# Optimization experiments

Hardware: AMD Instinct MI355X
Metric: run time of the kernel (lower is better)

The kernel has to match this reference:

```python
import jax, jax.numpy as jnp
import numpy as np

N_TOKENS = 65536
HIDDEN = 1024
N_EXPERTS = 64
EPS = 1e-12  # matches F.normalize default eps
NEG_BIG = float(jnp.finfo(jnp.bfloat16).max)  # -torch.finfo(bfloat16).max sentinel


def setup_inputs() -> dict:
    key = jax.random.key(0)
    k1, k2 = jax.random.split(key)
    x = jax.random.normal(k1, (N_TOKENS, HIDDEN), dtype=jnp.float32)
    sim_matrix = jax.random.normal(k2, (HIDDEN, N_EXPERTS), dtype=jnp.float32)  # nn.Parameter(randn)
    gates = jnp.zeros((N_EXPERTS,), dtype=jnp.float32)  # nn.Parameter(zeros)
    return {"x": x, "sim_matrix": sim_matrix, "gates": gates}


def _l2norm(v, axis):
    n = jnp.sqrt(jnp.sum(v * v, axis=axis, keepdims=True))
    return v / jnp.maximum(n, EPS)


def reference(x, sim_matrix, gates):
    # cosine-similarity logits: [N, E]
    logits = jnp.matmul(_l2norm(x, -1), _l2norm(sim_matrix, 0))
    thr = jax.nn.sigmoid(gates)                      # [E]
    pre_activation_logits = logits - thr             # [N, E]
    gated = jax.nn.relu(pre_activation_logits)
    # STE: forward hard 0/1, backward identity
    hard = (gated > 0).astype(x.dtype)
    activation_mask = gated + jax.lax.stop_gradient(hard - gated)
    # topk fallback for rows with zero active experts (vectorized scatter)
    inactive = jnp.sum(hard, axis=1) == 0            # [N]
    k_fallback = N_EXPERTS // 2
    _, topk_idx = jax.lax.top_k(logits, k_fallback)  # [N, k]
    rows = jnp.arange(x.shape[0])
    fb = jnp.zeros_like(logits).at[rows[:, None], topk_idx].set(1.0)
    activation_mask = jnp.where(inactive[:, None], fb, activation_mask)
    # masked softmax over active experts
    masked = jnp.where(activation_mask > 0, gated, -NEG_BIG)
    active_expert_probs = jax.nn.softmax(masked, axis=-1)
    return active_expert_probs, pre_activation_logits, activation_mask
```

## Files before the change

kernel.cpp:

```cpp
#include <hip/hip_runtime.h>
#include <math.h>

#define N_TOK   65536
#define HID     1024
#define NEXP    64
#define EPSF    1e-12f
#define EPSW    4e-5f

typedef __attribute__((ext_vector_type(8))) short s16x8;
typedef __attribute__((ext_vector_type(4))) float f32x4;

__device__ __forceinline__ unsigned short f2bf(float f) {
    unsigned u = __float_as_uint(f);
    unsigned r = u + 0x7fffu + ((u >> 16) & 1u);
    return (unsigned short)(r >> 16);
}
__device__ __forceinline__ float bf2f(unsigned short h) {
    return __uint_as_float(((unsigned)h) << 16);
}
__device__ __forceinline__ unsigned enc_key(float f) {
    unsigned u = __float_as_uint(f);
    return (u & 0x80000000u) ? ~u : (u | 0x80000000u);
}
__device__ __forceinline__ float dec_key(unsigned k) {
    unsigned u = (k & 0x80000000u) ? (k ^ 0x80000000u) : ~k;
    return __uint_as_float(u);
}

__global__ __launch_bounds__(256) void prep_kernel(const float* __restrict__ sim,
                                                   const float* __restrict__ gates,
                                                   float* __restrict__ ws) {
    __shared__ float partial[4][64];
    int e = threadIdx.x & 63;
    int q = threadIdx.x >> 6;
    float s = 0.f;
    for (int h = q * 256; h < q * 256 + 256; ++h) {
        float v = sim[h * NEXP + e];
        s += v * v;
    }
    partial[q][e] = s;
    __syncthreads();
    if (threadIdx.x < 64) {
        float ss = partial[0][e] + partial[1][e] + partial[2][e] + partial[3][e];
        ws[e] = 1.0f / fmaxf(sqrtf(ss), EPSF);
        ws[64 + e] = 1.0f / (1.0f + expf(-gates[e]));
    }
}

__global__ __launch_bounds__(256) void prep2n_kernel(const float* __restrict__ sim,
                                                     const float* __restrict__ ws_ro,
                                                     float* __restrict__ wn) {
    int idx = blockIdx.x * 256 + threadIdx.x;
    wn[idx] = sim[idx] * ws_ro[idx & 63];
}

__global__ __launch_bounds__(256) void prep3_kernel(const float* __restrict__ wn,
                                                    unsigned short* __restrict__ wbh,
                                                    unsigned short* __restrict__ wbl) {
    int i = blockIdx.x * 256 + threadIdx.x;
    int j    = i & 7;
    int lane = (i >> 3) & 63;
    int nt   = (i >> 9) & 3;
    int kt   = i >> 11;
    int k = kt * 32 + ((lane >> 4) & 3) * 8 + j;
    int e = nt * 16 + (lane & 15);
    float v = wn[k * NEXP + e];
    unsigned short h = f2bf(v);
    unsigned short l = f2bf(v - bf2f(h));
    wbh[i] = h; wbl[i] = l;
}

__global__ __launch_bounds__(256) void gate_v11_kernel(const float* __restrict__ x,
                                                       const float* __restrict__ wn,
                                                       const unsigned short* __restrict__ wbh,
                                                       const unsigned short* __restrict__ wbl,
                                                       const float* __restrict__ prep,
                                                       float* __restrict__ out) {
    __shared__ __align__(16) float smem[6016];
    float* xrow    = smem + 4352;
    float* ss_part = smem + 5376;
    float* thr_l   = smem + 5632;
    int*   flags_i = (int*)(smem + 5696);
    float* part    = smem + 5760;
    unsigned short* AhU = (unsigned short*)smem;
    unsigned short* AlU = (unsigned short*)(smem + 2080);

    const int tid   = threadIdx.x;
    const int lane  = tid & 63;
    const int wv    = tid >> 6;
    const int tbase = blockIdx.x * 64;

    const int t_st = tid & 63;
    const int q_st = tid >> 6;
    const int fl   = (t_st & 15) + 16 * q_st;
    const int mt   = t_st >> 4;
    const float* xrow_g = x + (size_t)(tbase + t_st) * HID;

    if (tid < 64) thr_l[tid] = prep[64 + tid];

    f32x4 acc[4];
#pragma unroll
    for (int m = 0; m < 4; ++m) acc[m] = (f32x4){0.f, 0.f, 0.f, 0.f};
    float ss = 0.f;

    const s16x8* bh_g = (const s16x8*)wbh;
    const s16x8* bl_g = (const s16x8*)wbl;

    {
        float4 v0 = *(const float4*)(xrow_g + q_st * 8);
        float4 v1 = *(const float4*)(xrow_g + q_st * 8 + 4);
        const float a[8] = { v0.x, v0.y, v0.z, v0.w, v1.x, v1.y, v1.z, v1.w };
        s16x8 hv, lv;
#pragma unroll
        for (int i = 0; i < 8; ++i) {
            ss = fmaf(a[i], a[i], ss);
            unsigned short h = f2bf(a[i]);
            hv[i] = (short)h;
            lv[i] = (short)f2bf(a[i] - bf2f(h));
        }
        int slot = mt * 65 + fl;
        *(s16x8*)&AhU[slot * 8] = hv;
        *(s16x8*)&AlU[slot * 8] = lv;
    }
    s16x8 bh = bh_g[(0 * 4 + wv) * 64 + lane];
    s16x8 bl = bl_g[(0 * 4 + wv) * 64 + lane];
    __syncthreads();

#pragma unroll 1
    for (int c = 0; c < 32; ++c) {
        const int buf = c & 1;
        float4 nv0, nv1;
        s16x8 nbh, nbl;
        if (c < 31) {
            nv0 = *(const float4*)(xrow_g + (c + 1) * 32 + q_st * 8);
            nv1 = *(const float4*)(xrow_g + (c + 1) * 32 + q_st * 8 + 4);
            nbh = bh_g[((c + 1) * 4 + wv) * 64 + lane];
            nbl = bl_g[((c + 1) * 4 + wv) * 64 + lane];
        }

        s16x8 ah[4], al[4];
#pragma unroll
        for (int m = 0; m < 4; ++m) {
            int base = ((buf << 2) + m) * 65 * 8 + lane * 8;
            ah[m] = *(const s16x8*)&AhU[base];
            al[m] = *(const s16x8*)&AlU[base];
        }
#pragma unroll
        for (int m = 0; m < 4; ++m)
            acc[m] = __builtin_amdgcn_mfma_f32_16x16x32_bf16(al[m], bh, acc[m], 0, 0, 0);
#pragma unroll
        for (int m = 0; m < 4; ++m)
            acc[m] = __builtin_amdgcn_mfma_f32_16x16x32_bf16(ah[m], bl, acc[m], 0, 0, 0);
#pragma unroll
        for (int m = 0; m < 4; ++m)
            acc[m] = __builtin_amdgcn_mfma_f32_16x16x32_bf16(ah[m], bh, acc[m], 0, 0, 0);

        if (c < 31) {
            const float a[8] = { nv0.x, nv0.y, nv0.z, nv0.w, nv1.x, nv1.y, nv1.z, nv1.w };
            s16x8 hv, lv;
#pragma unroll
            for (int i = 0; i < 8; ++i) {
                ss = fmaf(a[i], a[i], ss);
                unsigned short h = f2bf(a[i]);
                hv[i] = (short)h;
                lv[i] = (short)f2bf(a[i] - bf2f(h));
            }
            int slot = (((buf ^ 1) << 2) + mt) * 65 + fl;
            *(s16x8*)&AhU[slot * 8] = hv;
            *(s16x8*)&AlU[slot * 8] = lv;
            bh = nbh; bl = nbl;
        }
        __syncthreads();
    }

    ss_part[q_st * 64 + t_st] = ss;
    {
        float* lg = smem;
#pragma unroll
        for (int m = 0; m < 4; ++m) {
#pragma unroll
            for (int r = 0; r < 4; ++r) {
                int tok = m * 16 + (lane >> 4) * 4 + r;
                int e   = wv * 16 + (lane & 15);
                lg[tok * 68 + e] = acc[m][r];
            }
        }
    }
    __syncthreads();

    const int tg = lane >> 3;
    const int eg = lane & 7;
    const int e0 = eg * 8;
    const size_t out_pre  = (size_t)N_TOK * NEXP;
    const size_t out_mask = 2 * (size_t)N_TOK * NEXP;

#pragma unroll
    for (int j = 0; j < 2; ++j) {
        const int tl = wv * 16 + tg * 2 + j;
        const int t  = tbase + tl;
        const float sst = (ss_part[tl] + ss_part[64 + tl])
                        + (ss_part[128 + tl] + ss_part[192 + tl]);
        const float inv = 1.0f / fmaxf(sqrtf(sst), EPSF);

        float logit[8], pre[8];
        int active[8];
        int myact = 0;
#pragma unroll
        for (int i = 0; i < 8; ++i) {
            logit[i] = smem[tl * 68 + e0 + i] * inv;
            pre[i]   = logit[i] - thr_l[e0 + i];
            active[i] = pre[i] > 0.f;
            myact += active[i];
        }
        *(float4*)&out[out_pre + (size_t)t * NEXP + e0]     = make_float4(pre[0], pre[1], pre[2], pre[3]);
        *(float4*)&out[out_pre + (size_t)t * NEXP + e0 + 4] = make_float4(pre[4], pre[5], pre[6], pre[7]);

        int rowact = myact;
        rowact += __shfl_xor(rowact, 1, 8);
        rowact += __shfl_xor(rowact, 2, 8);
        rowact += __shfl_xor(rowact, 4, 8);

        int flag;
        if (rowact > 0) {
            float mn = 1e30f;
#pragma unroll
            for (int i = 0; i < 8; ++i) mn = fminf(mn, fabsf(pre[i]));
            mn = fminf(mn, __shfl_xor(mn, 1, 8));
            mn = fminf(mn, __shfl_xor(mn, 2, 8));
            mn = fminf(mn, __shfl_xor(mn, 4, 8));
            flag = (mn <= EPSW);
            if (!flag) {
                float gated[8], probs[8], mask[8];
#pragma unroll
                for (int i = 0; i < 8; ++i) gated[i] = fmaxf(pre[i], 0.f);
                float m = -INFINITY;
#pragma unroll
                for (int i = 0; i < 8; ++i) m = fmaxf(m, active[i] ? gated[i] : -INFINITY);
                m = fmaxf(m, __shfl_xor(m, 1, 8));
                m = fmaxf(m, __shfl_xor(m, 2, 8));
                m = fmaxf(m, __shfl_xor(m, 4, 8));
                float s = 0.f;
#pragma unroll
                for (int i = 0; i < 8; ++i) {
                    float ev = active[i] ? expf(gated[i] - m) : 0.f;
                    probs[i] = ev; s += ev;
                }
                s += __shfl_xor(s, 1, 8);
                s += __shfl_xor(s, 2, 8);
                s += __shfl_xor(s, 4, 8);
                float rs = 1.0f / s;
#pragma unroll
                for (int i = 0; i < 8; ++i) { probs[i] *= rs; mask[i] = active[i] ? 1.f : 0.f; }
                size_t row = (size_t)t * NEXP + e0;
                *(float4*)&out[row]                = make_float4(probs[0], probs[1], probs[2], probs[3]);
                *(float4*)&out[row + 4]            = make_float4(probs[4], probs[5], probs[6], probs[7]);
                *(float4*)&out[out_mask + row]     = make_float4(mask[0], mask[1], mask[2], mask[3]);
                *(float4*)&out[out_mask + row + 4] = make_float4(mask[4], mask[5], mask[6], mask[7]);
            }
        } else {
            unsigned key[8];
#pragma unroll
            for (int i = 0; i < 8; ++i) key[i] = enc_key(logit[i]);
            unsigned cand = 0u;
            for (int bit = 31; bit >= 0; --bit) {
                unsigned test = cand | (1u << bit);
                int c = 0;
#pragma unroll
                for (int i = 0; i < 8; ++i) c += (key[i] >= test);
                c += __shfl_xor(c, 1, 8);
                c += __shfl_xor(c, 2, 8);
                c += __shfl_xor(c, 4, 8);
                if (c >= 32) cand = test;
            }
            const float val32 = dec_key(cand);
            int nhi = 0, nlo = 0, nam = 0;
#pragma unroll
            for (int i = 0; i < 8; ++i) {
                nhi += logit[i] > val32 + EPSW;
                nlo += logit[i] > val32 - EPSW;
                nam += pre[i] > -EPSW;
            }
            nhi += __shfl_xor(nhi, 1, 8); nhi += __shfl_xor(nhi, 2, 8); nhi += __shfl_xor(nhi, 4, 8);
            nlo += __shfl_xor(nlo, 1, 8); nlo += __shfl_xor(nlo, 2, 8); nlo += __shfl_xor(nlo, 4, 8);
            nam += __shfl_xor(nam, 1, 8); nam += __shfl_xor(nam, 2, 8); nam += __shfl_xor(nam, 4, 8);
            flag = !(nhi == 31 && nlo == 32) || (nam > 0);
            if (!flag) {
                float probs[8], mask[8];
#pragma unroll
                for (int i = 0; i < 8; ++i) {
                    int sel = logit[i] > val32 - EPSW;
                    mask[i]  = sel ? 1.f : 0.f;
                    probs[i] = sel ? 0.03125f : 0.f;
                }
                size_t row = (size_t)t * NEXP + e0;
                *(float4*)&out[row]                = make_float4(probs[0], probs[1], probs[2], probs[3]);
                *(float4*)&out[row + 4]            = make_float4(probs[4], probs[5], probs[6], probs[7]);
                *(float4*)&out[out_mask + row]     = make_float4(mask[0], mask[1], mask[2], mask[3]);
                *(float4*)&out[out_mask + row + 4] = make_float4(mask[4], mask[5], mask[6], mask[7]);
            }
        }
        if (eg == 0) flags_i[tl] = flag;
    }
    __syncthreads();

    for (int tf = 0; tf < 64; ++tf) {
        if (flags_i[tf] == 0) continue;
        {
            float4 v = *(const float4*)&x[(size_t)(tbase + tf) * HID + tid * 4];
            *(float4*)&xrow[tid * 4] = v;
        }
        __syncthreads();
        const int e = tid & 63;
        const int q = tid >> 6;
        const float* wp = wn + (size_t)q * 256 * NEXP + e;
        const float* xr = xrow + q * 256;
        float dot = 0.f;
#pragma unroll 8
        for (int k2 = 0; k2 < 256; ++k2)
            dot = fmaf(xr[k2], wp[(size_t)k2 * NEXP], dot);
        part[q * 64 + e] = dot;
        __syncthreads();
        if (tid < 64) {
            const float sst = (ss_part[tf] + ss_part[64 + tf])
                            + (ss_part[128 + tf] + ss_part[192 + tf]);
            const float inv = 1.0f / fmaxf(sqrtf(sst), EPSF);
            const float lg = ((part[e] + part[64 + e]) + (part[128 + e] + part[192 + e])) * inv;
            const float pr = lg - thr_l[e];
            unsigned long long act = __ballot(pr > 0.f);
            float probs, mask;
            if (act) {
                float g = fmaxf(pr, 0.f);
                float mv = (pr > 0.f) ? g : -INFINITY;
#pragma unroll
                for (int d = 1; d < 64; d <<= 1) mv = fmaxf(mv, __shfl_xor(mv, d));
                float ex = (pr > 0.f) ? expf(g - mv) : 0.f;
                float s = ex;
#pragma unroll
                for (int d = 1; d < 64; d <<= 1) s += __shfl_xor(s, d);
                probs = ex / s;
                mask  = (pr > 0.f) ? 1.f : 0.f;
            } else {
                unsigned key = enc_key(lg);
                unsigned cand = 0u;
                for (int bit = 31; bit >= 0; --bit) {
                    unsigned test = cand | (1u << bit);
                    int c = __popcll(__ballot(key >= test));
                    if (c >= 32) cand = test;
                }
                int need = 32 - __popcll(__ballot(key > cand));
                unsigned long long em = __ballot(key == cand);
                unsigned long long mlt = e ? (~0ull >> (64 - e)) : 0ull;
                int below = __popcll(em & mlt);
                int sel = (key > cand) || ((key == cand) && (below < need));
                probs = sel ? 0.03125f : 0.f;
                mask  = sel ? 1.f : 0.f;
            }
            size_t row = (size_t)(tbase + tf) * NEXP;
            out[row + e] = probs;
            out[out_mask + row + e] = mask;
        }
        __syncthreads();
    }
}

__global__ __launch_bounds__(256) void gate_v10_kernel(const float* __restrict__ x,
                                                       const float* __restrict__ wn,
                                                       const float* __restrict__ prep,
                                                       float* __restrict__ out) {
    __shared__ __align__(16) float smem[8704];
    float* ss_part = smem + 8448;
    const int tid  = threadIdx.x;
    const int lane = tid & 63;
    const int wv   = tid >> 6;
    const int tg   = lane >> 3;
    const int eg   = lane & 7;
    const int e0   = eg * 8;
    const int tbase = blockIdx.x * 64;
    const int kbase = wv * 256;
    float* xsw = smem + wv * 2112;
    const float4* xq4 = (const float4*)(x + (size_t)(tbase + lane) * HID + kbase);
    float acc[8][8];
#pragma unroll
    for (int t = 0; t < 8; ++t)
#pragma unroll
        for (int e = 0; e < 8; ++e) acc[t][e] = 0.f;
    float ss = 0.f;
    {
        float4 f0 = xq4[0], f1 = xq4[1];
        const float4* wq4 = (const float4*)(wn + (size_t)kbase * NEXP) + lane * 2;
        float4 w0 = wq4[0], w1 = wq4[1];
        const float a[8] = { f0.x, f0.y, f0.z, f0.w, f1.x, f1.y, f1.z, f1.w };
#pragma unroll
        for (int i = 0; i < 8; ++i) { ss = fmaf(a[i], a[i], ss); xsw[i * 68 + lane] = a[i]; }
        *(float4*)&xsw[1088 + lane * 8]     = w0;
        *(float4*)&xsw[1088 + lane * 8 + 4] = w1;
    }
#define FMA8x8(XA, XB, WA, WB)                                              \
    do {                                                                    \
        const float xv_[8] = { XA.x, XA.y, XA.z, XA.w, XB.x, XB.y, XB.z, XB.w }; \
        const float wv_[8] = { WA.x, WA.y, WA.z, WA.w, WB.x, WB.y, WB.z, WB.w }; \
        _Pragma("unroll")                                                   \
        for (int t_ = 0; t_ < 8; ++t_)                                      \
            _Pragma("unroll")                                               \
            for (int e_ = 0; e_ < 8; ++e_)                                  \
                acc[t_][e_] = fmaf(xv_[t_], wv_[e_], acc[t_][e_]);          \
    } while (0)
#pragma unroll 1
    for (int c = 0; c < 32; ++c) {
        float4 sx0, sx1, sw0, sw1;
        if (c < 31) {
            sx0 = xq4[(c + 1) * 2];
            sx1 = xq4[(c + 1) * 2 + 1];
            const float4* wq4 = (const float4*)(wn + (size_t)(kbase + (c + 1) * 8) * NEXP) + lane * 2;
            sw0 = wq4[0]; sw1 = wq4[1];
        }
        const float* xb = xsw + (c & 1) * 544;
        const float* wb = xsw + 1088 + (c & 1) * 512;
#pragma unroll
        for (int k = 0; k < 8; ++k) {
            const float4 xa = *(const float4*)&xb[k * 68 + tg * 8];
            const float4 xc = *(const float4*)&xb[k * 68 + tg * 8 + 4];
            const float4 wa = *(const float4*)&wb[k * 64 + e0];
            const float4 wc = *(const float4*)&wb[k * 64 + e0 + 4];
            FMA8x8(xa, xc, wa, wc);
        }
        if (c < 31) {
            float* xn = xsw + ((c + 1) & 1) * 544;
            float* wl = xsw + 1088 + ((c + 1) & 1) * 512;
            const float a[8] = { sx0.x, sx0.y, sx0.z, sx0.w, sx1.x, sx1.y, sx1.z, sx1.w };
#pragma unroll
            for (int i = 0; i < 8; ++i) { ss = fmaf(a[i], a[i], ss); xn[i * 68 + lane] = a[i]; }
            *(float4*)&wl[lane * 8]     = sw0;
            *(float4*)&wl[lane * 8 + 4] = sw1;
        }
    }
#undef FMA8x8
    ss_part[wv * 64 + lane] = ss;
    __syncthreads();
    if (wv < 2) {
        float* reg = smem + wv * 4224;
#pragma unroll
        for (int j = 0; j < 8; ++j) {
            float* p = &reg[(tg * 8 + j) * 65 + e0];
            *(float4*)(p)     = make_float4(acc[j][0], acc[j][1], acc[j][2], acc[j][3]);
            *(float4*)(p + 4) = make_float4(acc[j][4], acc[j][5], acc[j][6], acc[j][7]);
        }
    }
    __syncthreads();
    if (wv >= 2) {
        float* reg = smem + (wv - 2) * 4224;
#pragma unroll
        for (int j = 0; j < 8; ++j) {
            float* p = &reg[(tg * 8 + j) * 65 + e0];
            float4 p0 = *(const float4*)(p);
            float4 p1 = *(const float4*)(p + 4);
            p0.x += acc[j][0]; p0.y += acc[j][1]; p0.z += acc[j][2]; p0.w += acc[j][3];
            p1.x += acc[j][4]; p1.y += acc[j][5]; p1.z += acc[j][6]; p1.w += acc[j][7];
            *(float4*)(p) = p0; *(float4*)(p + 4) = p1;
        }
    }
    __syncthreads();
    float thr[8];
#pragma unroll
    for (int i = 0; i < 8; ++i) thr[i] = prep[64 + e0 + i];
    const size_t out_pre  = (size_t)N_TOK * NEXP;
    const size_t out_mask = 2 * (size_t)N_TOK * NEXP;
    const float* regA = smem;
    const float* regB = smem + 4224;
#pragma unroll
    for (int j = 0; j < 2; ++j) {
        const int tl = wv * 16 + tg * 2 + j;
        const int t  = tbase + tl;
        const float sst = (ss_part[tl] + ss_part[64 + tl]) + (ss_part[128 + tl] + ss_part[192 + tl]);
        const float inv = 1.0f / fmaxf(sqrtf(sst), EPSF);
        float4 aA0 = *(const float4*)&regA[tl * 65 + e0];
        float4 aA1 = *(const float4*)&regA[tl * 65 + e0 + 4];
        float4 aB0 = *(const float4*)&regB[tl * 65 + e0];
        float4 aB1 = *(const float4*)&regB[tl * 65 + e0 + 4];
        float logit[8] = { (aA0.x + aB0.x) * inv, (aA0.y + aB0.y) * inv,
                           (aA0.z + aB0.z) * inv, (aA0.w + aB0.w) * inv,
                           (aA1.x + aB1.x) * inv, (aA1.y + aB1.y) * inv,
                           (aA1.z + aB1.z) * inv, (aA1.w + aB1.w) * inv };
        float pre[8], gated[8];
        int active[8];
        int myact = 0;
#pragma unroll
        for (int i = 0; i < 8; ++i) {
            pre[i]   = logit[i] - thr[i];
            gated[i] = fmaxf(pre[i], 0.f);
            active[i] = pre[i] > 0.f;
            myact += active[i];
        }
        int rowact = myact;
        rowact += __shfl_xor(rowact, 1, 8);
        rowact += __shfl_xor(rowact, 2, 8);
        rowact += __shfl_xor(rowact, 4, 8);
        float probs[8], mask[8];
        if (rowact > 0) {
            float m = -INFINITY;
#pragma unroll
            for (int i = 0; i < 8; ++i) m = fmaxf(m, active[i] ? gated[i] : -INFINITY);
            m = fmaxf(m, __shfl_xor(m, 1, 8));
            m = fmaxf(m, __shfl_xor(m, 2, 8));
            m = fmaxf(m, __shfl_xor(m, 4, 8));
            float s = 0.f;
#pragma unroll
            for (int i = 0; i < 8; ++i) { float ev = active[i] ? expf(gated[i] - m) : 0.f; probs[i] = ev; s += ev; }
            s += __shfl_xor(s, 1, 8);
            s += __shfl_xor(s, 2, 8);
            s += __shfl_xor(s, 4, 8);
            float rs = 1.0f / s;
#pragma unroll
            for (int i = 0; i < 8; ++i) { probs[i] *= rs; mask[i] = active[i] ? 1.f : 0.f; }
        } else {
            unsigned key[8];
#pragma unroll
            for (int i = 0; i < 8; ++i) key[i] = enc_key(logit[i]);
            unsigned cand = 0u;
            for (int bit = 31; bit >= 0; --bit) {
                unsigned test = cand | (1u << bit);
                int c = 0;
#pragma unroll
                for (int i = 0; i < 8; ++i) c += (key[i] >= test);
                c += __shfl_xor(c, 1, 8);
                c += __shfl_xor(c, 2, 8);
                c += __shfl_xor(c, 4, 8);
                if (c >= 32) cand = test;
            }
            int cgt = 0;
#pragma unroll
            for (int i = 0; i < 8; ++i) cgt += (key[i] > cand);
            cgt += __shfl_xor(cgt, 1, 8);
            cgt += __shfl_xor(cgt, 2, 8);
            cgt += __shfl_xor(cgt, 4, 8);
            int need_eq = 32 - cgt;
            int eqc = 0;
#pragma unroll
            for (int i = 0; i < 8; ++i) eqc += (key[i] == cand);
            int scan = eqc, tmp;
            tmp = __shfl_up(scan, 1, 8); if (eg >= 1) scan += tmp;
            tmp = __shfl_up(scan, 2, 8); if (eg >= 2) scan += tmp;
            tmp = __shfl_up(scan, 4, 8); if (eg >= 4) scan += tmp;
            int run = scan - eqc;
#pragma unroll
            for (int i = 0; i < 8; ++i) {
                int sel = (key[i] > cand) || ((key[i] == cand) && (run < need_eq));
                run += (key[i] == cand);
                mask[i]  = sel ? 1.f : 0.f;
                probs[i] = sel ? 0.03125f : 0.f;
            }
        }
        const size_t row = (size_t)t * NEXP + e0;
        *(float4*)&out[row]                = make_float4(probs[0], probs[1], probs[2], probs[3]);
        *(float4*)&out[row + 4]            = make_float4(probs[4], probs[5], probs[6], probs[7]);
        *(float4*)&out[out_pre + row]      = make_float4(pre[0], pre[1], pre[2], pre[3]);
        *(float4*)&out[out_pre + row + 4]  = make_float4(pre[4], pre[5], pre[6], pre[7]);
        *(float4*)&out[out_mask + row]     = make_float4(mask[0], mask[1], mask[2], mask[3]);
        *(float4*)&out[out_mask + row + 4] = make_float4(mask[4], mask[5], mask[6], mask[7]);
    }
}

#define TOKB    128
#define KC      64
#define XPAD    65
__global__ __launch_bounds__(256) void gate_kernel_fb(const float* __restrict__ x,
                                                      const float* __restrict__ sim,
                                                      const float* __restrict__ prep,
                                                      float* __restrict__ out) {
    __shared__ float x_lds[TOKB][XPAD];
    __shared__ float w_lds[KC][NEXP];
    __shared__ float ss_lds[TOKB];
    __shared__ float invcol[NEXP];
    __shared__ float thr_s[NEXP];
    const int tid = threadIdx.x;
    const int base_t = blockIdx.x * TOKB;
    if (tid < NEXP) { invcol[tid] = prep[tid]; thr_s[tid] = prep[64 + tid]; }
    if (tid < TOKB) ss_lds[tid] = 0.f;
    const int g_e = tid & 7;
    const int g_t = tid >> 3;
    const int e0 = g_e * 8;
    const int t0 = g_t * 4;
    const int lt = tid >> 4;
    const int lk = (tid & 15) * 4;
    float acc[4][8];
#pragma unroll
    for (int j = 0; j < 4; ++j)
#pragma unroll
        for (int i = 0; i < 8; ++i) acc[j][i] = 0.f;
    for (int kc = 0; kc < HID; kc += KC) {
        __syncthreads();
#pragma unroll
        for (int it = 0; it < 4; ++it) {
            int flat4 = it * 256 + tid;
            int k = flat4 >> 4;
            int e = (flat4 & 15) * 4;
            float4 v = *(const float4*)&sim[(size_t)(kc + k) * NEXP + e];
            v.x *= invcol[e]; v.y *= invcol[e + 1]; v.z *= invcol[e + 2]; v.w *= invcol[e + 3];
            *(float4*)&w_lds[k][e] = v;
        }
#pragma unroll
        for (int it = 0; it < 8; ++it) {
            int t = it * 16 + lt;
            float4 v = *(const float4*)&x[(size_t)(base_t + t) * HID + kc + lk];
            x_lds[t][lk + 0] = v.x; x_lds[t][lk + 1] = v.y;
            x_lds[t][lk + 2] = v.z; x_lds[t][lk + 3] = v.w;
            float s4 = v.x * v.x + v.y * v.y + v.z * v.z + v.w * v.w;
            s4 += __shfl_xor(s4, 1, 16);
            s4 += __shfl_xor(s4, 2, 16);
            s4 += __shfl_xor(s4, 4, 16);
            s4 += __shfl_xor(s4, 8, 16);
            if ((tid & 15) == 0) ss_lds[t] += s4;
        }
        __syncthreads();
#pragma unroll 8
        for (int k = 0; k < KC; ++k) {
            float x0 = x_lds[t0 + 0][k];
            float x1 = x_lds[t0 + 1][k];
            float x2 = x_lds[t0 + 2][k];
            float x3 = x_lds[t0 + 3][k];
            float4 w0 = *(const float4*)&w_lds[k][e0];
            float4 w1 = *(const float4*)&w_lds[k][e0 + 4];
            float wv[8] = { w0.x, w0.y, w0.z, w0.w, w1.x, w1.y, w1.z, w1.w };
#pragma unroll
            for (int i = 0; i < 8; ++i) {
                acc[0][i] += x0 * wv[i];
                acc[1][i] += x1 * wv[i];
                acc[2][i] += x2 * wv[i];
                acc[3][i] += x3 * wv[i];
            }
        }
    }
    const size_t out_pre  = (size_t)N_TOK * NEXP;
    const size_t out_mask = 2 * (size_t)N_TOK * NEXP;
#pragma unroll
    for (int j = 0; j < 4; ++j) {
        int t = t0 + j;
        float inv = 1.0f / fmaxf(sqrtf(ss_lds[t]), EPSF);
        float logit[8], pre[8], gated[8];
        int active[8];
        int myact = 0;
#pragma unroll
        for (int i = 0; i < 8; ++i) {
            logit[i] = acc[j][i] * inv;
            pre[i]   = logit[i] - thr_s[e0 + i];
            gated[i] = fmaxf(pre[i], 0.f);
            active[i] = pre[i] > 0.f;
            myact += active[i];
        }
        int rowact = myact;
        rowact += __shfl_xor(rowact, 1, 8);
        rowact += __shfl_xor(rowact, 2, 8);
        rowact += __shfl_xor(rowact, 4, 8);
        float probs[8], mask[8];
        if (rowact > 0) {
            float m = -INFINITY;
#pragma unroll
            for (int i = 0; i < 8; ++i) m = fmaxf(m, active[i] ? gated[i] : -INFINITY);
            m = fmaxf(m, __shfl_xor(m, 1, 8));
            m = fmaxf(m, __shfl_xor(m, 2, 8));
            m = fmaxf(m, __shfl_xor(m, 4, 8));
            float s = 0.f;
#pragma unroll
            for (int i = 0; i < 8; ++i) { float ev = active[i] ? expf(gated[i] - m) : 0.f; probs[i] = ev; s += ev; }
            s += __shfl_xor(s, 1, 8);
            s += __shfl_xor(s, 2, 8);
            s += __shfl_xor(s, 4, 8);
            float rs = 1.0f / s;
#pragma unroll
            for (int i = 0; i < 8; ++i) { probs[i] *= rs; mask[i] = active[i] ? 1.f : 0.f; }
        } else {
            unsigned key[8];
#pragma unroll
            for (int i = 0; i < 8; ++i) key[i] = enc_key(logit[i]);
            unsigned cand = 0u;
            for (int bit = 31; bit >= 0; --bit) {
                unsigned test = cand | (1u << bit);
                int c = 0;
#pragma unroll
                for (int i = 0; i < 8; ++i) c += (key[i] >= test);
                c += __shfl_xor(c, 1, 8);
                c += __shfl_xor(c, 2, 8);
                c += __shfl_xor(c, 4, 8);
                if (c >= 32) cand = test;
            }
            int cgt = 0;
#pragma unroll
            for (int i = 0; i < 8; ++i) cgt += (key[i] > cand);
            cgt += __shfl_xor(cgt, 1, 8);
            cgt += __shfl_xor(cgt, 2, 8);
            cgt += __shfl_xor(cgt, 4, 8);
            int need_eq = 32 - cgt;
            int eqc = 0;
#pragma unroll
            for (int i = 0; i < 8; ++i) eqc += (key[i] == cand);
            int scan = eqc, tmp;
            tmp = __shfl_up(scan, 1, 8); if (g_e >= 1) scan += tmp;
            tmp = __shfl_up(scan, 2, 8); if (g_e >= 2) scan += tmp;
            tmp = __shfl_up(scan, 4, 8); if (g_e >= 4) scan += tmp;
            int run = scan - eqc;
#pragma unroll
            for (int i = 0; i < 8; ++i) {
                int sel = (key[i] > cand) || ((key[i] == cand) && (run < need_eq));
                run += (key[i] == cand);
                mask[i]  = sel ? 1.f : 0.f;
                probs[i] = sel ? 0.03125f : 0.f;
            }
        }
        size_t row = (size_t)(base_t + t) * NEXP + e0;
        *(float4*)&out[row]                = make_float4(probs[0], probs[1], probs[2], probs[3]);
        *(float4*)&out[row + 4]            = make_float4(probs[4], probs[5], probs[6], probs[7]);
        *(float4*)&out[out_pre + row]      = make_float4(pre[0], pre[1], pre[2], pre[3]);
        *(float4*)&out[out_pre + row + 4]  = make_float4(pre[4], pre[5], pre[6], pre[7]);
        *(float4*)&out[out_mask + row]     = make_float4(mask[0], mask[1], mask[2], mask[3]);
        *(float4*)&out[out_mask + row + 4] = make_float4(mask[4], mask[5], mask[6], mask[7]);
    }
}

extern "C" void kernel_launch(void* const* d_in, const int* in_sizes, int n_in,
                              void* d_out, int out_size, void* d_ws, size_t ws_size,
                              hipStream_t stream) {
    (void)in_sizes; (void)n_in; (void)out_size;
    const float* x     = (const float*)d_in[0];
    const float* sim   = (const float*)d_in[1];
    const float* gates = (const float*)d_in[2];
    float* out = (float*)d_out;
    float* ws  = (float*)d_ws;

    hipLaunchKernelGGL(prep_kernel, dim3(1), dim3(256), 0, stream, sim, gates, ws);

    const size_t need_v10 = 512 + (size_t)HID * NEXP * sizeof(float);
    const size_t need_v11 = need_v10 + 2 * (size_t)HID * NEXP * sizeof(short);
    if (ws_size >= need_v11) {
        float* wn = ws + 128;
        unsigned short* wbh = (unsigned short*)(ws + 128 + HID * NEXP / 1);
        wbh = (unsigned short*)((char*)ws + 512 + (size_t)HID * NEXP * 4);
        unsigned short* wbl = wbh + (size_t)HID * NEXP;
        hipLaunchKernelGGL(prep2n_kernel, dim3(HID * NEXP / 256), dim3(256), 0, stream,
                           sim, ws, wn);
        hipLaunchKernelGGL(prep3_kernel, dim3(HID * NEXP / 256), dim3(256), 0, stream,
                           wn, wbh, wbl);
        hipLaunchKernelGGL(gate_v11_kernel, dim3(N_TOK / 64), dim3(256), 0, stream,
                           x, wn, wbh, wbl, ws, out);
    } else if (ws_size >= need_v10) {
        float* wn = ws + 128;
        hipLaunchKernelGGL(prep2n_kernel, dim3(HID * NEXP / 256), dim3(256), 0, stream,
                           sim, ws, wn);
        hipLaunchKernelGGL(gate_v10_kernel, dim3(N_TOK / 64), dim3(256), 0, stream,
                           x, wn, ws, out);
    } else {
        hipLaunchKernelGGL(gate_kernel_fb, dim3(N_TOK / TOKB), dim3(256), 0, stream,
                           x, sim, ws, out);
    }
}
```

Before: 190.1 us.

## Load A fragments directly from global per wave, dropping LDS staging and barriers

Reassigns the MFMA work so each wave owns 16 tokens across all 64 experts. Each lane loads its own x fragment from global straight into registers, which removes the per-chunk LDS writes and reads of the split bf16 A tiles and the __syncthreads in the K loop. The cost is that each wave now loads all four B tiles (hi and lo) per chunk, raising L2 traffic and register pressure, and the x load pattern becomes strided per lane. The fp32 fallback kernel is also removed.

```diff
diff --git a/kernel.cpp b/kernel.cpp
--- a/kernel.cpp
+++ b/kernel.cpp
@@ -70,122 +70,84 @@
     wbh[i] = h; wbl[i] = l;
 }
 
-__global__ __launch_bounds__(256) void gate_v11_kernel(const float* __restrict__ x,
+__global__ __launch_bounds__(256) void gate_v12_kernel(const float* __restrict__ x,
                                                        const float* __restrict__ wn,
                                                        const unsigned short* __restrict__ wbh,
                                                        const unsigned short* __restrict__ wbl,
                                                        const float* __restrict__ prep,
                                                        float* __restrict__ out) {
-    __shared__ __align__(16) float smem[6016];
-    float* xrow    = smem + 4352;
-    float* ss_part = smem + 5376;
-    float* thr_l   = smem + 5632;
-    int*   flags_i = (int*)(smem + 5696);
-    float* part    = smem + 5760;
-    unsigned short* AhU = (unsigned short*)smem;
-    unsigned short* AlU = (unsigned short*)(smem + 2080);
+    __shared__ __align__(16) float lg[64][68];
+    __shared__ __align__(16) float xrow[HID];
+    __shared__ float ss_l[64];
+    __shared__ float thr_l[64];
+    __shared__ int   flags_i[64];
+    __shared__ float part[256];
 
     const int tid   = threadIdx.x;
     const int lane  = tid & 63;
     const int wv    = tid >> 6;
     const int tbase = blockIdx.x * 64;
 
-    const int t_st = tid & 63;
-    const int q_st = tid >> 6;
-    const int fl   = (t_st & 15) + 16 * q_st;
-    const int mt   = t_st >> 4;
-    const float* xrow_g = x + (size_t)(tbase + t_st) * HID;
+    const int arow = lane & 15;
+    const int aoct = lane >> 4;
+    const float* xg = x + (size_t)(tbase + wv * 16 + arow) * HID + aoct * 8;
 
     if (tid < 64) thr_l[tid] = prep[64 + tid];
 
     f32x4 acc[4];
 #pragma unroll
-    for (int m = 0; m < 4; ++m) acc[m] = (f32x4){0.f, 0.f, 0.f, 0.f};
+    for (int nt = 0; nt < 4; ++nt) acc[nt] = (f32x4){0.f, 0.f, 0.f, 0.f};
     float ss = 0.f;
 
     const s16x8* bh_g = (const s16x8*)wbh;
     const s16x8* bl_g = (const s16x8*)wbl;
 
-    {
-        float4 v0 = *(const float4*)(xrow_g + q_st * 8);
-        float4 v1 = *(const float4*)(xrow_g + q_st * 8 + 4);
-        const float a[8] = { v0.x, v0.y, v0.z, v0.w, v1.x, v1.y, v1.z, v1.w };
-        s16x8 hv, lv;
+    float4 xv0 = *(const float4*)(xg);
+    float4 xv1 = *(const float4*)(xg + 4);
+
+#pragma unroll 2
+    for (int c = 0; c < 32; ++c) {
+        float4 nx0, nx1;
+        if (c < 31) {
+            nx0 = *(const float4*)(xg + (c + 1) * 32);
+            nx1 = *(const float4*)(xg + (c + 1) * 32 + 4);
+        }
+        s16x8 bh[4], bl[4];
+#pragma unroll
+        for (int nt = 0; nt < 4; ++nt) {
+            bh[nt] = bh_g[(c * 4 + nt) * 64 + lane];
+            bl[nt] = bl_g[(c * 4 + nt) * 64 + lane];
+        }
+        const float a[8] = { xv0.x, xv0.y, xv0.z, xv0.w, xv1.x, xv1.y, xv1.z, xv1.w };
+        s16x8 ah, al;
 #pragma unroll
         for (int i = 0; i < 8; ++i) {
             ss = fmaf(a[i], a[i], ss);
             unsigned short h = f2bf(a[i]);
-            hv[i] = (short)h;
-            lv[i] = (short)f2bf(a[i] - bf2f(h));
-        }
-        int slot = mt * 65 + fl;
-        *(s16x8*)&AhU[slot * 8] = hv;
-        *(s16x8*)&AlU[slot * 8] = lv;
-    }
-    s16x8 bh = bh_g[(0 * 4 + wv) * 64 + lane];
-    s16x8 bl = bl_g[(0 * 4 + wv) * 64 + lane];
-    __syncthreads();
-
-#pragma unroll 1
-    for (int c = 0; c < 32; ++c) {
-        const int buf = c & 1;
-        float4 nv0, nv1;
-        s16x8 nbh, nbl;
-        if (c < 31) {
-            nv0 = *(const float4*)(xrow_g + (c + 1) * 32 + q_st * 8);
-            nv1 = *(const float4*)(xrow_g + (c + 1) * 32 + q_st * 8 + 4);
-            nbh = bh_g[((c + 1) * 4 + wv) * 64 + lane];
-            nbl = bl_g[((c + 1) * 4 + wv) * 64 + lane];
-        }
-
-        s16x8 ah[4], al[4];
-#pragma unroll
-        for (int m = 0; m < 4; ++m) {
-            int base = ((buf << 2) + m) * 65 * 8 + lane * 8;
-            ah[m] = *(const s16x8*)&AhU[base];
-            al[m] = *(const s16x8*)&AlU[base];
-        }
-#pragma unroll
-        for (int m = 0; m < 4; ++m)
-            acc[m] = __builtin_amdgcn_mfma_f32_16x16x32_bf16(al[m], bh, acc[m], 0, 0, 0);
-#pragma unroll
-        for (int m = 0; m < 4; ++m)
-            acc[m] = __builtin_amdgcn_mfma_f32_16x16x32_bf16(ah[m], bl, acc[m], 0, 0, 0);
-#pragma unroll
-        for (int m = 0; m < 4; ++m)
-            acc[m] = __builtin_amdgcn_mfma_f32_16x16x32_bf16(ah[m], bh, acc[m], 0, 0, 0);
-
-        if (c < 31) {
-            const float a[8] = { nv0.x, nv0.y, nv0.z, nv0.w, nv1.x, nv1.y, nv1.z, nv1.w };
-            s16x8 hv, lv;
-#pragma unroll
-            for (int i = 0; i < 8; ++i) {
-                ss = fmaf(a[i], a[i], ss);
-                unsigned short h = f2bf(a[i]);
-                hv[i] = (short)h;
-                lv[i] = (short)f2bf(a[i] - bf2f(h));
-            }
-            int slot = (((buf ^ 1) << 2) + mt) * 65 + fl;
-            *(s16x8*)&AhU[slot * 8] = hv;
-            *(s16x8*)&AlU[slot * 8] = lv;
-            bh = nbh; bl = nbl;
-        }
-        __syncthreads();
-    }
-
-    ss_part[q_st * 64 + t_st] = ss;
-    {
-        float* lg = smem;
-#pragma unroll
-        for (int m = 0; m < 4; ++m) {
-#pragma unroll
-            for (int r = 0; r < 4; ++r) {
-                int tok = m * 16 + (lane >> 4) * 4 + r;
-                int e   = wv * 16 + (lane & 15);
-                lg[tok * 68 + e] = acc[m][r];
-            }
-        }
-    }
+            ah[i] = (short)h;
+            al[i] = (short)f2bf(a[i] - bf2f(h));
+        }
+#pragma unroll
+        for (int nt = 0; nt < 4; ++nt)
+            acc[nt] = __builtin_amdgcn_mfma_f32_16x16x32_bf16(al, bh[nt], acc[nt], 0, 0, 0);
+#pragma unroll
+        for (int nt = 0; nt < 4; ++nt)
+            acc[nt] = __builtin_amdgcn_mfma_f32_16x16x32_bf16(ah, bl[nt], acc[nt], 0, 0, 0);
+#pragma unroll
+        for (int nt = 0; nt < 4; ++nt)
+            acc[nt] = __builtin_amdgcn_mfma_f32_16x16x32_bf16(ah, bh[nt], acc[nt], 0, 0, 0);
+        xv0 = nx0; xv1 = nx1;
+    }
+
+    ss += __shfl_xor(ss, 16);
+    ss += __shfl_xor(ss, 32);
+    if (lane < 16) ss_l[wv * 16 + lane] = ss;
+
+#pragma unroll
+    for (int nt = 0; nt < 4; ++nt)
+#pragma unroll
+        for (int r = 0; r < 4; ++r)
+            lg[wv * 16 + aoct * 4 + r][nt * 16 + arow] = acc[nt][r];
     __syncthreads();
 
     const int tg = lane >> 3;
@@ -198,16 +160,14 @@
     for (int j = 0; j < 2; ++j) {
         const int tl = wv * 16 + tg * 2 + j;
         const int t  = tbase + tl;
-        const float sst = (ss_part[tl] + ss_part[64 + tl])
-                        + (ss_part[128 + tl] + ss_part[192 + tl]);
-        const float inv = 1.0f / fmaxf(sqrtf(sst), EPSF);
+        const float inv = 1.0f / fmaxf(sqrtf(ss_l[tl]), EPSF);
 
         float logit[8], pre[8];
         int active[8];
         int myact = 0;
 #pragma unroll
         for (int i = 0; i < 8; ++i) {
-            logit[i] = smem[tl * 68 + e0 + i] * inv;
+            logit[i] = lg[tl][e0 + i] * inv;
             pre[i]   = logit[i] - thr_l[e0 + i];
             active[i] = pre[i] > 0.f;
             myact += active[i];
@@ -321,11 +281,9 @@
         part[q * 64 + e] = dot;
         __syncthreads();
         if (tid < 64) {
-            const float sst = (ss_part[tf] + ss_part[64 + tf])
-                            + (ss_part[128 + tf] + ss_part[192 + tf]);
-            const float inv = 1.0f / fmaxf(sqrtf(sst), EPSF);
-            const float lg = ((part[e] + part[64 + e]) + (part[128 + e] + part[192 + e])) * inv;
-            const float pr = lg - thr_l[e];
+            const float inv = 1.0f / fmaxf(sqrtf(ss_l[tf]), EPSF);
+            const float lgv = ((part[e] + part[64 + e]) + (part[128 + e] + part[192 + e])) * inv;
+            const float pr = lgv - thr_l[e];
             unsigned long long act = __ballot(pr > 0.f);
             float probs, mask;
             if (act) {
@@ -340,7 +298,7 @@
                 probs = ex / s;
                 mask  = (pr > 0.f) ? 1.f : 0.f;
             } else {
-                unsigned key = enc_key(lg);
+                unsigned key = enc_key(lgv);
                 unsigned cand = 0u;
                 for (int bit = 31; bit >= 0; --bit) {
                     unsigned test = cand | (1u << bit);
@@ -560,162 +518,6 @@
     }
 }
 
-#define TOKB    128
-#define KC      64
-#define XPAD    65
-__global__ __launch_bounds__(256) void gate_kernel_fb(const float* __restrict__ x,
-                                                      const float* __restrict__ sim,
-                                                      const float* __restrict__ prep,
-                                                      float* __restrict__ out) {
-    __shared__ float x_lds[TOKB][XPAD];
-    __shared__ float w_lds[KC][NEXP];
-    __shared__ float ss_lds[TOKB];
-    __shared__ float invcol[NEXP];
-    __shared__ float thr_s[NEXP];
-    const int tid = threadIdx.x;
-    const int base_t = blockIdx.x * TOKB;
-    if (tid < NEXP) { invcol[tid] = prep[tid]; thr_s[tid] = prep[64 + tid]; }
-    if (tid < TOKB) ss_lds[tid] = 0.f;
-    const int g_e = tid & 7;
-    const int g_t = tid >> 3;
-    const int e0 = g_e * 8;
-    const int t0 = g_t * 4;
-    const int lt = tid >> 4;
-    const int lk = (tid & 15) * 4;
-    float acc[4][8];
-#pragma unroll
-    for (int j = 0; j < 4; ++j)
-#pragma unroll
-        for (int i = 0; i < 8; ++i) acc[j][i] = 0.f;
-    for (int kc = 0; kc < HID; kc += KC) {
-        __syncthreads();
-#pragma unroll
-        for (int it = 0; it < 4; ++it) {
-            int flat4 = it * 256 + tid;
-            int k = flat4 >> 4;
-            int e = (flat4 & 15) * 4;
-            float4 v = *(const float4*)&sim[(size_t)(kc + k) * NEXP + e];
-            v.x *= invcol[e]; v.y *= invcol[e + 1]; v.z *= invcol[e + 2]; v.w *= invcol[e + 3];
-            *(float4*)&w_lds[k][e] = v;
-        }
-#pragma unroll
-        for (int it = 0; it < 8; ++it) {
-            int t = it * 16 + lt;
-            float4 v = *(const float4*)&x[(size_t)(base_t + t) * HID + kc + lk];
-            x_lds[t][lk + 0] = v.x; x_lds[t][lk + 1] = v.y;
-            x_lds[t][lk + 2] = v.z; x_lds[t][lk + 3] = v.w;
-            float s4 = v.x * v.x + v.y * v.y + v.z * v.z + v.w * v.w;
-            s4 += __shfl_xor(s4, 1, 16);
-            s4 += __shfl_xor(s4, 2, 16);
-            s4 += __shfl_xor(s4, 4, 16);
-            s4 += __shfl_xor(s4, 8, 16);
-            if ((tid & 15) == 0) ss_lds[t] += s4;
-        }
-        __syncthreads();
-#pragma unroll 8
-        for (int k = 0; k < KC; ++k) {
-            float x0 = x_lds[t0 + 0][k];
-            float x1 = x_lds[t0 + 1][k];
-            float x2 = x_lds[t0 + 2][k];
-            float x3 = x_lds[t0 + 3][k];
-            float4 w0 = *(const float4*)&w_lds[k][e0];
-            float4 w1 = *(const float4*)&w_lds[k][e0 + 4];
-            float wv[8] = { w0.x, w0.y, w0.z, w0.w, w1.x, w1.y, w1.z, w1.w };
-#pragma unroll
-            for (int i = 0; i < 8; ++i) {
-                acc[0][i] += x0 * wv[i];
-                acc[1][i] += x1 * wv[i];
-                acc[2][i] += x2 * wv[i];
-                acc[3][i] += x3 * wv[i];
-            }
-        }
-    }
-    const size_t out_pre  = (size_t)N_TOK * NEXP;
-    const size_t out_mask = 2 * (size_t)N_TOK * NEXP;
-#pragma unroll
-    for (int j = 0; j < 4; ++j) {
-        int t = t0 + j;
-        float inv = 1.0f / fmaxf(sqrtf(ss_lds[t]), EPSF);
-        float logit[8], pre[8], gated[8];
-        int active[8];
-        int myact = 0;
-#pragma unroll
-        for (int i = 0; i < 8; ++i) {
-            logit[i] = acc[j][i] * inv;
-            pre[i]   = logit[i] - thr_s[e0 + i];
-            gated[i] = fmaxf(pre[i], 0.f);
-            active[i] = pre[i] > 0.f;
-            myact += active[i];
-        }
-        int rowact = myact;
-        rowact += __shfl_xor(rowact, 1, 8);
-        rowact += __shfl_xor(rowact, 2, 8);
-        rowact += __shfl_xor(rowact, 4, 8);
-        float probs[8], mask[8];
-        if (rowact > 0) {
-            float m = -INFINITY;
-#pragma unroll
-            for (int i = 0; i < 8; ++i) m = fmaxf(m, active[i] ? gated[i] : -INFINITY);
-            m = fmaxf(m, __shfl_xor(m, 1, 8));
-            m = fmaxf(m, __shfl_xor(m, 2, 8));
-            m = fmaxf(m, __shfl_xor(m, 4, 8));
-            float s = 0.f;
-#pragma unroll
-            for (int i = 0; i < 8; ++i) { float ev = active[i] ? expf(gated[i] - m) : 0.f; probs[i] = ev; s += ev; }
-            s += __shfl_xor(s, 1, 8);
-            s += __shfl_xor(s, 2, 8);
-            s += __shfl_xor(s, 4, 8);
-            float rs = 1.0f / s;
-#pragma unroll
-            for (int i = 0; i < 8; ++i) { probs[i] *= rs; mask[i] = active[i] ? 1.f : 0.f; }
-        } else {
-            unsigned key[8];
-#pragma unroll
-            for (int i = 0; i < 8; ++i) key[i] = enc_key(logit[i]);
-            unsigned cand = 0u;
-            for (int bit = 31; bit >= 0; --bit) {
-                unsigned test = cand | (1u << bit);
-                int c = 0;
-#pragma unroll
-                for (int i = 0; i < 8; ++i) c += (key[i] >= test);
-                c += __shfl_xor(c, 1, 8);
-                c += __shfl_xor(c, 2, 8);
-                c += __shfl_xor(c, 4, 8);
-                if (c >= 32) cand = test;
-            }
-            int cgt = 0;
-#pragma unroll
-            for (int i = 0; i < 8; ++i) cgt += (key[i] > cand);
-            cgt += __shfl_xor(cgt, 1, 8);
-            cgt += __shfl_xor(cgt, 2, 8);
-            cgt += __shfl_xor(cgt, 4, 8);
-            int need_eq = 32 - cgt;
-            int eqc = 0;
-#pragma unroll
-            for (int i = 0; i < 8; ++i) eqc += (key[i] == cand);
-            int scan = eqc, tmp;
-            tmp = __shfl_up(scan, 1, 8); if (g_e >= 1) scan += tmp;
-            tmp = __shfl_up(scan, 2, 8); if (g_e >= 2) scan += tmp;
-            tmp = __shfl_up(scan, 4, 8); if (g_e >= 4) scan += tmp;
-            int run = scan - eqc;
-#pragma unroll
-            for (int i = 0; i < 8; ++i) {
-                int sel = (key[i] > cand) || ((key[i] == cand) && (run < need_eq));
-                run += (key[i] == cand);
-                mask[i]  = sel ? 1.f : 0.f;
-                probs[i] = sel ? 0.03125f : 0.f;
-            }
-        }
-        size_t row = (size_t)(base_t + t) * NEXP + e0;
-        *(float4*)&out[row]                = make_float4(probs[0], probs[1], probs[2], probs[3]);
-        *(float4*)&out[row + 4]            = make_float4(probs[4], probs[5], probs[6], probs[7]);
-        *(float4*)&out[out_pre + row]      = make_float4(pre[0], pre[1], pre[2], pre[3]);
-        *(float4*)&out[out_pre + row + 4]  = make_float4(pre[4], pre[5], pre[6], pre[7]);
-        *(float4*)&out[out_mask + row]     = make_float4(mask[0], mask[1], mask[2], mask[3]);
-        *(float4*)&out[out_mask + row + 4] = make_float4(mask[4], mask[5], mask[6], mask[7]);
-    }
-}
-
 extern "C" void kernel_launch(void* const* d_in, const int* in_sizes, int n_in,
                               void* d_out, int out_size, void* d_ws, size_t ws_size,
                               hipStream_t stream) {
@@ -729,26 +531,22 @@
     hipLaunchKernelGGL(prep_kernel, dim3(1), dim3(256), 0, stream, sim, gates, ws);
 
     const size_t need_v10 = 512 + (size_t)HID * NEXP * sizeof(float);
-    const size_t need_v11 = need_v10 + 2 * (size_t)HID * NEXP * sizeof(short);
-    if (ws_size >= need_v11) {
+    const size_t need_v12 = need_v10 + 2 * (size_t)HID * NEXP * sizeof(short);
+    if (ws_size >= need_v12) {
         float* wn = ws + 128;
-        unsigned short* wbh = (unsigned short*)(ws + 128 + HID * NEXP / 1);
-        wbh = (unsigned short*)((char*)ws + 512 + (size_t)HID * NEXP * 4);
+        unsigned short* wbh = (unsigned short*)((char*)ws + 512 + (size_t)HID * NEXP * 4);
         unsigned short* wbl = wbh + (size_t)HID * NEXP;
         hipLaunchKernelGGL(prep2n_kernel, dim3(HID * NEXP / 256), dim3(256), 0, stream,
                            sim, ws, wn);
         hipLaunchKernelGGL(prep3_kernel, dim3(HID * NEXP / 256), dim3(256), 0, stream,
                            wn, wbh, wbl);
-        hipLaunchKernelGGL(gate_v11_kernel, dim3(N_TOK / 64), dim3(256), 0, stream,
+        hipLaunchKernelGGL(gate_v12_kernel, dim3(N_TOK / 64), dim3(256), 0, stream,
                            x, wn, wbh, wbl, ws, out);
-    } else if (ws_size >= need_v10) {
+    } else {
         float* wn = ws + 128;
         hipLaunchKernelGGL(prep2n_kernel, dim3(HID * NEXP / 256), dim3(256), 0, stream,
                            sim, ws, wn);
         hipLaunchKernelGGL(gate_v10_kernel, dim3(N_TOK / 64), dim3(256), 0, stream,
                            x, wn, ws, out);
-    } else {
-        hipLaunchKernelGGL(gate_kernel_fb, dim3(N_TOK / TOKB), dim3(256), 0, stream,
-                           x, sim, ws, out);
-    }
-}
+    }
+}
```

Result: slower. 197.0 us (+3.6%).
